# Kernel tuning notes

Measured on AMD Instinct MI355X. Metric: run time of the kernel, lower is better.

The kernel has to match this reference:

```python
import jax, jax.numpy as jnp
import numpy as np

DIM = 256
M = 100000
B = 1024
TOP_K = 32
N_HEADS = 4
EPS = 1e-8  # torch F.cosine_similarity eps


def setup_inputs() -> dict:
    key = jax.random.key(0)
    ks = jax.random.split(key, 8)
    return {
        "query": jax.random.normal(ks[0], (B, DIM), dtype=jnp.float32),
        "mem_keys": jax.random.normal(ks[1], (M, DIM), dtype=jnp.float32),
        "mem_values": jax.random.normal(ks[2], (M, DIM), dtype=jnp.float32),
        "W_q": jax.random.normal(ks[3], (DIM, DIM), dtype=jnp.float32) * 0.1,
        "in_proj_w": jax.random.normal(ks[4], (3 * DIM, DIM), dtype=jnp.float32) * 0.05,
        "in_proj_b": jax.random.normal(ks[5], (3 * DIM,), dtype=jnp.float32) * 0.05,
        "out_proj_w": jax.random.normal(ks[6], (DIM, DIM), dtype=jnp.float32) * 0.05,
        "out_proj_b": jax.random.normal(ks[7], (DIM,), dtype=jnp.float32) * 0.05,
    }


def reference(query, mem_keys, mem_values, W_q, in_proj_w, in_proj_b, out_proj_w, out_proj_b):
    b, d = query.shape
    hd = d // N_HEADS

    # projected query used both for retrieval and as attention query
    qt = query @ W_q  # [B, D]

    # batched cosine similarity against the whole bank
    qn = qt / jnp.maximum(jnp.linalg.norm(qt, axis=-1, keepdims=True), EPS)
    kn = mem_keys / jnp.maximum(jnp.linalg.norm(mem_keys, axis=-1, keepdims=True), EPS)
    sims = qn @ kn.T  # [B, M]  -- memory-bound stage

    _, idx = jax.lax.top_k(sims, TOP_K)  # [B, K]
    rk = mem_keys[idx]    # [B, K, D]
    rv = mem_values[idx]  # [B, K, D]

    # nn.MultiheadAttention math (batch_first, q_len=1, kv_len=K)
    Wq, Wk, Wv = jnp.split(in_proj_w, 3, axis=0)
    bq, bk, bv = jnp.split(in_proj_b, 3)
    q = qt @ Wq.T + bq                # [B, D]
    k = rk @ Wk.T + bk                # [B, K, D]
    v = rv @ Wv.T + bv                # [B, K, D]

    qh = q.reshape(b, N_HEADS, hd)                      # [B, H, hd]
    kh = k.reshape(b, TOP_K, N_HEADS, hd)               # [B, K, H, hd]
    vh = v.reshape(b, TOP_K, N_HEADS, hd)

    scores = jnp.einsum('bhd,bkhd->bhk', qh, kh) / jnp.sqrt(jnp.float32(hd))
    attn = jax.nn.softmax(scores, axis=-1)              # [B, H, K]
    out = jnp.einsum('bhk,bkhd->bhd', attn, vh).reshape(b, d)
    return out @ out_proj_w.T + out_proj_b              # [B, D]
```

## Files before the change

kernel.cpp:

```cpp
#include <hip/hip_runtime.h>
#include <hip/hip_bf16.h>

#define BQ 1024
#define DIMD 256
#define MKEYS 100000
#define TOPK 32
#define NSUPER 3125
#define PAIR_CAP 1024
#define EBUF_CAP 320
#define WKOFF (DIMD * DIMD)
#define WVOFF (2 * DIMD * DIMD)

typedef __attribute__((ext_vector_type(8))) short bf16x8;
typedef __attribute__((ext_vector_type(4))) float f32x4;

#define MFMA_16x16x32(a, b, c) __builtin_amdgcn_mfma_f32_16x16x32_bf16(a, b, c, 0, 0, 0)

__global__ __launch_bounds__(256) void k_zero(int* __restrict__ cnt) {
    const int i = blockIdx.x * 256 + threadIdx.x;
    if (i < BQ) cnt[i] = 0;
}

__global__ __launch_bounds__(256) void k_qt(const float* __restrict__ query,
                                            const float* __restrict__ Wq,
                                            float* __restrict__ qt,
                                            __hip_bfloat16* __restrict__ qtb,
                                            float* __restrict__ emit_thr) {
    __shared__ float qrow[DIMD];
    __shared__ float red[256];
    const int b = blockIdx.x, t = threadIdx.x;
    qrow[t] = query[b * DIMD + t];
    __syncthreads();
    float acc = 0.f;
#pragma unroll 4
    for (int k = 0; k < DIMD; ++k)
        acc = fmaf(qrow[k], Wq[k * DIMD + t], acc);
    qt[b * DIMD + t] = acc;
    qtb[b * DIMD + t] = __float2bfloat16(acc);
    red[t] = acc * acc;
    __syncthreads();
    for (int s = 128; s > 0; s >>= 1) {
        if (t < s) red[t] += red[t + s];
        __syncthreads();
    }
    if (t == 0) {
        const float sigma = sqrtf(red[0]) * (1.0f / 16.0f);
        emit_thr[b] = 3.0f * sigma - 0.02f;
    }
}

__global__ __launch_bounds__(256) void k_kn(const float* __restrict__ keys,
                                            __hip_bfloat16* __restrict__ knb,
                                            float* __restrict__ invn) {
    const int wv = threadIdx.x >> 6, lane = threadIdx.x & 63;
    const int row = blockIdx.x * 4 + wv;
    const float4 v = *(const float4*)(keys + (size_t)row * DIMD + lane * 4);
    float ss = v.x * v.x + v.y * v.y + v.z * v.z + v.w * v.w;
#pragma unroll
    for (int m = 1; m < 64; m <<= 1) ss += __shfl_xor(ss, m);
    const float inv = 1.0f / fmaxf(sqrtf(ss), 1e-8f);
    ushort4 u;
    u.x = (unsigned short)__builtin_bit_cast(short, __float2bfloat16(v.x * inv));
    u.y = (unsigned short)__builtin_bit_cast(short, __float2bfloat16(v.y * inv));
    u.z = (unsigned short)__builtin_bit_cast(short, __float2bfloat16(v.z * inv));
    u.w = (unsigned short)__builtin_bit_cast(short, __float2bfloat16(v.w * inv));
    *(ushort4*)((unsigned short*)knb + (size_t)row * DIMD + lane * 4) = u;
    if (lane == 0) invn[row] = inv;
}

__global__ __launch_bounds__(256) void k_tr(const float* __restrict__ in_w,
                                            const float* __restrict__ ow,
                                            float* __restrict__ wqT,
                                            float* __restrict__ owT) {
    __shared__ float tile[32][33];
    const int m = blockIdx.z;
    const float* src = (m == 0) ? in_w : ow;
    float* dst = (m == 0) ? wqT : owT;
    const int r0 = blockIdx.y * 32, c0 = blockIdx.x * 32;
    const int tr = threadIdx.x >> 5, tc = threadIdx.x & 31;
#pragma unroll
    for (int i = 0; i < 32; i += 8)
        tile[tr + i][tc] = src[(size_t)(r0 + tr + i) * DIMD + c0 + tc];
    __syncthreads();
#pragma unroll
    for (int i = 0; i < 32; i += 8)
        dst[(size_t)(c0 + tr + i) * DIMD + r0 + tc] = tile[tc][tr + i];
}

__global__ __launch_bounds__(256) void k_comb(const float* __restrict__ in_w,
                                              const float* __restrict__ in_b,
                                              const float* __restrict__ ob,
                                              const float* __restrict__ wqT,
                                              const float* __restrict__ owT,
                                              float* __restrict__ CombG,
                                              float* __restrict__ gbias,
                                              float* __restrict__ CombO,
                                              float* __restrict__ obias) {
    const int t = threadIdx.x;
    const int bid = blockIdx.x;
    if (bid < 256) {
        __shared__ float qe[DIMD];
        qe[t] = wqT[bid * DIMD + t];
        __syncthreads();
#pragma unroll
        for (int h = 0; h < 4; ++h) {
            float acc = 0.f;
#pragma unroll 4
            for (int d = 0; d < 64; ++d)
                acc = fmaf(qe[h * 64 + d], in_w[WKOFF + (size_t)(h * 64 + d) * DIMD + t], acc);
            CombG[(size_t)bid * 1024 + h * 256 + t] = acc;
        }
    } else if (bid < 1280) {
        const int hc = bid - 256;
        const int h = hc >> 8, c = hc & 255;
        float acc = 0.f;
#pragma unroll 4
        for (int d = 0; d < 64; ++d) {
            const int tt = h * 64 + d;
            acc = fmaf(in_w[WVOFF + (size_t)tt * DIMD + c], owT[(size_t)tt * DIMD + t], acc);
        }
        CombO[(size_t)hc * DIMD + t] = acc;
    } else if (bid == 1280) {
#pragma unroll
        for (int h = 0; h < 4; ++h) {
            float acc = 0.f;
#pragma unroll 4
            for (int d = 0; d < 64; ++d)
                acc = fmaf(in_b[h * 64 + d], in_w[WKOFF + (size_t)(h * 64 + d) * DIMD + t], acc);
            gbias[h * 256 + t] = acc;
        }
    } else {
        float acc = ob[t];
#pragma unroll 4
        for (int tt = 0; tt < DIMD; ++tt)
            acc = fmaf(in_b[2 * DIMD + tt], owT[(size_t)tt * DIMD + t], acc);
        obias[t] = acc;
    }
}

__global__ __launch_bounds__(256, 3) void k_sims(const __hip_bfloat16* __restrict__ qtb,
                                                 const __hip_bfloat16* __restrict__ knb,
                                                 const float* __restrict__ emit_thr,
                                                 int* __restrict__ cnt,
                                                 int2* __restrict__ pairs)
{
    __shared__ __align__(16) unsigned char btile[32 * 512];
    __shared__ float sthr[128];
    __shared__ int epack[EBUF_CAP];
    __shared__ float escore[EBUF_CAP];
    __shared__ int ebc;

    const int t = threadIdx.x;
    const int lane = t & 63;
    const int wv = t >> 6;
    const int col = lane & 15;
    const int quad = lane >> 4;
    const int xch = blockIdx.x >> 3;
    const int ych = blockIdx.x & 7;
    const int row0 = ych * 128;
    const int rloc_base = wv * 32;

    if (t < 128) sthr[t] = emit_thr[row0 + t];
    if (t == 0) ebc = 0;
    __syncthreads();

    float thr[2][4];
#pragma unroll
    for (int sub = 0; sub < 2; ++sub)
#pragma unroll
        for (int reg = 0; reg < 4; ++reg)
            thr[sub][reg] = sthr[rloc_base + sub * 16 + quad * 4 + reg];

    bf16x8 afr[2][8];
#pragma unroll
    for (int sub = 0; sub < 2; ++sub) {
        const short* ap = (const short*)qtb + (size_t)(row0 + rloc_base + sub * 16 + col) * DIMD;
#pragma unroll
        for (int kk = 0; kk < 8; ++kk)
            afr[sub][kk] = *(const bf16x8*)(ap + kk * 32 + quad * 8);
    }

    const int fm = t & 31;
    const int fr0 = t >> 5;

    const int st0 = xch * 25;
    const int st1 = st0 + 25;

    bf16x8 stg[4];
    {
        const char* gp = (const char*)knb + (size_t)st0 * 32 * 512;
#pragma unroll
        for (int it = 0; it < 4; ++it) {
            const int r = it * 8 + fr0;
            stg[it] = *(const bf16x8*)(gp + r * 512 + fm * 16);
        }
    }

    for (int st = st0; st < st1; ++st) {
        __syncthreads();
#pragma unroll
        for (int it = 0; it < 4; ++it) {
            const int r = it * 8 + fr0;
            *(bf16x8*)(btile + r * 512 + ((fm ^ (r & 7)) * 16)) = stg[it];
        }
        __syncthreads();

        if (st + 1 < st1) {
            const char* gp = (const char*)knb + (size_t)(st + 1) * 32 * 512;
#pragma unroll
            for (int it = 0; it < 4; ++it) {
                const int r = it * 8 + fr0;
                stg[it] = *(const bf16x8*)(gp + r * 512 + fm * 16);
            }
        }

        const int c0 = st * 32;
        f32x4 acc[2][2];
#pragma unroll
        for (int i = 0; i < 2; ++i)
#pragma unroll
            for (int j = 0; j < 2; ++j) { acc[i][j][0] = 0.f; acc[i][j][1] = 0.f; acc[i][j][2] = 0.f; acc[i][j][3] = 0.f; }

#pragma unroll
        for (int kt = 0; kt < 2; ++kt) {
            const int n = kt * 16 + col;
            const unsigned char* bp = btile + n * 512;
            const int nx = n & 7;
#pragma unroll
            for (int kk = 0; kk < 8; ++kk) {
                const int m = kk * 4 + quad;
                const bf16x8 b = *(const bf16x8*)(bp + ((m ^ nx) * 16));
                acc[0][kt] = MFMA_16x16x32(afr[0][kk], b, acc[0][kt]);
                acc[1][kt] = MFMA_16x16x32(afr[1][kk], b, acc[1][kt]);
            }
        }

#pragma unroll
        for (int sub = 0; sub < 2; ++sub) {
#pragma unroll
            for (int kt = 0; kt < 2; ++kt) {
#pragma unroll
                for (int reg = 0; reg < 4; ++reg) {
                    const float s = acc[sub][kt][reg];
                    if (s >= thr[sub][reg]) {
                        const int rl = rloc_base + sub * 16 + quad * 4 + reg;
                        const int key = c0 + kt * 16 + col;
                        const int p = atomicAdd(&ebc, 1);
                        if (p < EBUF_CAP) {
                            epack[p] = (rl << 17) | key;
                            escore[p] = s;
                        }
                    }
                }
            }
        }
    }

    __syncthreads();
    const int ne = min(ebc, EBUF_CAP);
    for (int i = t; i < ne; i += 256) {
        const int pk = epack[i];
        const int row = row0 + (pk >> 17);
        const int key = pk & 0x1FFFF;
        const int p = atomicAdd(&cnt[row], 1);
        if (p < PAIR_CAP)
            pairs[(size_t)row * PAIR_CAP + p] = make_int2(key, __float_as_int(escore[i]));
    }
}

__global__ __launch_bounds__(256) void k_pick(const int* __restrict__ cnt,
                                              const int2* __restrict__ pairs,
                                              const float* __restrict__ qt,
                                              const float* __restrict__ keys,
                                              const float* __restrict__ invn,
                                              int* __restrict__ topk) {
    __shared__ float sval[PAIR_CAP];
    __shared__ int skey[PAIR_CAP];
    __shared__ float qs[DIMD];
    __shared__ float wex[64];
    __shared__ int widx[64];
    __shared__ int wcnt;
    __shared__ float t32s;

    const int t = threadIdx.x;
    const int row = blockIdx.x;
    const int wv = t >> 6, lane = t & 63;

    qs[t] = qt[row * DIMD + t];
    const int n = min(cnt[row], PAIR_CAP);
    for (int i = t; i < n; i += 256) {
        int2 p = pairs[(size_t)row * PAIR_CAP + i];
        skey[i] = p.x;
        sval[i] = __int_as_float(p.y);
    }
    if (t == 0) { wcnt = 0; t32s = -1e30f; }
    __syncthreads();

    const int target = min(31, n - 1);
    for (int i = t; i < n; i += 256) {
        const float v = sval[i];
        const int k = skey[i];
        int r = 0;
        for (int j = 0; j < n; ++j) {
            const float vj = sval[j];
            r += (vj > v) || (vj == v && skey[j] < k);
        }
        if (r == target) t32s = v;
    }
    __syncthreads();
    const float t32 = t32s;

    for (int i = t; i < n; i += 256)
        if (sval[i] >= t32 - 0.04f) {
            int p = atomicAdd(&wcnt, 1);
            if (p < 64) widx[p] = skey[i];
        }
    __syncthreads();
    const int wn = min(wcnt, 64);

    for (int c = wv; c < wn; c += 4) {
        const int key = widx[c];
        const float4 kv = ((const float4*)(keys + (size_t)key * DIMD))[lane];
        float s = kv.x * qs[lane * 4] + kv.y * qs[lane * 4 + 1] +
                  kv.z * qs[lane * 4 + 2] + kv.w * qs[lane * 4 + 3];
#pragma unroll
        for (int m = 1; m < 64; m <<= 1) s += __shfl_xor(s, m);
        if (lane == 0) wex[c] = s * invn[key];
    }
    __syncthreads();

    if (t < 64) {
        const bool have = t < wn;
        const float v = have ? wex[t] : -1e30f;
        const int k = have ? widx[t] : 0x7FFFFFFF;
        int r = 0;
        for (int j = 0; j < wn; ++j) {
            const float vj = wex[j];
            r += (vj > v) || (vj == v && widx[j] < k);
        }
        const bool sel = have && (r < TOPK);
        const unsigned long long mask = __ballot(sel);
        if (sel) {
            const int pos = __popcll(mask & ((1ull << t) - 1));
            topk[row * TOPK + pos] = k;
        }
        if (t == 0) {
            const int tot = __popcll(mask);
            for (int z = tot; z < TOPK; ++z) topk[row * TOPK + z] = 0;
        }
    }
}

__global__ __launch_bounds__(256) void k_g(const float* __restrict__ qt,
                                           const float* __restrict__ CombG,
                                           const float* __restrict__ gbias,
                                           float* __restrict__ G) {
    __shared__ __align__(16) float qts[8][264];
    const int t = threadIdx.x;
    const int b0 = blockIdx.x * 8;
    const int c0 = blockIdx.y * 512 + t;
    const int c1 = c0 + 256;

#pragma unroll
    for (int r = 0; r < 8; ++r) qts[r][t] = qt[(size_t)(b0 + r) * DIMD + t];
    __syncthreads();

    float acc0[8], acc1[8];
#pragma unroll
    for (int r = 0; r < 8; ++r) { acc0[r] = 0.f; acc1[r] = 0.f; }

    for (int e = 0; e < DIMD; e += 4) {
        float4 qf[8];
#pragma unroll
        for (int r = 0; r < 8; ++r) qf[r] = *(const float4*)&qts[r][e];
#pragma unroll
        for (int j = 0; j < 4; ++j) {
            const float w0 = CombG[(size_t)(e + j) * 1024 + c0];
            const float w1 = CombG[(size_t)(e + j) * 1024 + c1];
#pragma unroll
            for (int r = 0; r < 8; ++r) {
                const float qv = (j == 0) ? qf[r].x : (j == 1) ? qf[r].y : (j == 2) ? qf[r].z : qf[r].w;
                acc0[r] = fmaf(qv, w0, acc0[r]);
                acc1[r] = fmaf(qv, w1, acc1[r]);
            }
        }
    }

    const float gb0 = gbias[c0 & 1023];
    const float gb1 = gbias[c1 & 1023];
#pragma unroll
    for (int r = 0; r < 8; ++r) {
        G[(size_t)(b0 + r) * 1024 + c0] = acc0[r] + gb0;
        G[(size_t)(b0 + r) * 1024 + c1] = acc1[r] + gb1;
    }
}

__global__ __launch_bounds__(256) void k_att(const float* __restrict__ G,
                                             const float* __restrict__ mem_keys,
                                             const float* __restrict__ mem_values,
                                             const int* __restrict__ topk,
                                             float* __restrict__ rvbar) {
    __shared__ float gs[4 * DIMD];
    __shared__ __align__(16) float ktile[32 * 264];
    __shared__ float at[4][TOPK];

    const int t = threadIdx.x;
    const int b = blockIdx.x;
    const int gr = t >> 3, gc = t & 7;

    int idx = topk[b * TOPK + gr];
    idx = ((unsigned)idx < MKEYS) ? idx : 0;
    const float4* kp = (const float4*)(mem_keys + (size_t)idx * DIMD);
    const float4* vp = (const float4*)(mem_values + (size_t)idx * DIMD);

    float4 sk[8], sv[8];
#pragma unroll
    for (int i = 0; i < 8; ++i) sk[i] = kp[gc + 8 * i];
    const float4 g4 = ((const float4*)G)[(size_t)b * 256 + t];
#pragma unroll
    for (int i = 0; i < 8; ++i) sv[i] = vp[gc + 8 * i];

    ((float4*)gs)[t] = g4;
    {
        float* kd = ktile + gr * 264;
#pragma unroll
        for (int i = 0; i < 8; ++i)
            *(float4*)(kd + ((gc ^ (gr & 7)) + 8 * i) * 4) = sk[i];
    }
    __syncthreads();

    const int h = t >> 6;
    const int s = (t >> 1) & 31;
    const int half = t & 1;
    {
        const float* kr = ktile + s * 264;
        const float* gp = gs + h * DIMD + half * 128;
        float4 a4 = {0.f, 0.f, 0.f, 0.f};
#pragma unroll
        for (int j = 0; j < 32; ++j) {
            const int l = half * 32 + j;
            const int phys = ((l & 7) ^ (s & 7)) | (l & 56);
            const float4 kv = *(const float4*)(kr + phys * 4);
            const float4 gv = *(const float4*)(gp + j * 4);
            a4.x = fmaf(kv.x, gv.x, a4.x);
            a4.y = fmaf(kv.y, gv.y, a4.y);
            a4.z = fmaf(kv.z, gv.z, a4.z);
            a4.w = fmaf(kv.w, gv.w, a4.w);
        }
        float a = (a4.x + a4.y) + (a4.z + a4.w);
        a += __shfl_xor(a, 1);
        a *= 0.125f;
        float mx = a;
#pragma unroll
        for (int m = 32; m >= 1; m >>= 1) mx = fmaxf(mx, __shfl_xor(mx, m));
        const float e = __expf(a - mx);
        float sum = e;
#pragma unroll
        for (int m = 32; m >= 1; m >>= 1) sum += __shfl_xor(sum, m);
        at[h][s] = (e + e) / sum;
    }
    __syncthreads();

    {
        float* kd = ktile + gr * 264;
#pragma unroll
        for (int i = 0; i < 8; ++i)
            *(float4*)(kd + ((gc ^ (gr & 7)) + 8 * i) * 4) = sv[i];
    }
    __syncthreads();

    {
        float a0 = 0.f, a1 = 0.f, a2 = 0.f, a3 = 0.f;
        const int l = t >> 2, w = t & 3;
#pragma unroll
        for (int k = 0; k < TOPK; ++k) {
            const int phys = ((l & 7) ^ (k & 7)) | (l & 56);
            const float v = ktile[k * 264 + phys * 4 + w];
            a0 = fmaf(at[0][k], v, a0);
            a1 = fmaf(at[1][k], v, a1);
            a2 = fmaf(at[2][k], v, a2);
            a3 = fmaf(at[3][k], v, a3);
        }
        float* rp = rvbar + (size_t)b * 1024;
        rp[t] = a0;
        rp[256 + t] = a1;
        rp[512 + t] = a2;
        rp[768 + t] = a3;
    }
}

__global__ __launch_bounds__(256) void k_out(const float* __restrict__ rvbar,
                                             const float* __restrict__ CombO,
                                             const float* __restrict__ obias,
                                             float* __restrict__ out) {
    __shared__ __align__(16) float rvs[4][1024];
    const int t = threadIdx.x;
    const int b0 = blockIdx.x * 4;

#pragma unroll
    for (int r = 0; r < 4; ++r)
#pragma unroll
        for (int i = 0; i < 4; ++i)
            rvs[r][t + 256 * i] = rvbar[(size_t)(b0 + r) * 1024 + t + 256 * i];
    __syncthreads();

    float acc[4];
#pragma unroll
    for (int r = 0; r < 4; ++r) acc[r] = 0.f;

#pragma unroll 2
    for (int k = 0; k < 1024; k += 4) {
        float4 qf[4];
#pragma unroll
        for (int r = 0; r < 4; ++r) qf[r] = *(const float4*)&rvs[r][k];
#pragma unroll
        for (int j = 0; j < 4; ++j) {
            const float w = CombO[(size_t)(k + j) * DIMD + t];
#pragma unroll
            for (int r = 0; r < 4; ++r) {
                const float qv = (j == 0) ? qf[r].x : (j == 1) ? qf[r].y : (j == 2) ? qf[r].z : qf[r].w;
                acc[r] = fmaf(qv, w, acc[r]);
            }
        }
    }

    const float obt = obias[t];
#pragma unroll
    for (int r = 0; r < 4; ++r)
        out[(size_t)(b0 + r) * DIMD + t] = acc[r] + obt;
}

extern "C" void kernel_launch(void* const* d_in, const int* in_sizes, int n_in,
                              void* d_out, int out_size, void* d_ws, size_t ws_size,
                              hipStream_t stream) {
    const float* query = (const float*)d_in[0];
    const float* mem_keys = (const float*)d_in[1];
    const float* mem_values = (const float*)d_in[2];
    const float* Wq = (const float*)d_in[3];
    const float* in_w = (const float*)d_in[4];
    const float* in_b = (const float*)d_in[5];
    const float* ow = (const float*)d_in[6];
    const float* ob = (const float*)d_in[7];
    float* out = (float*)d_out;

    char* ws = (char*)d_ws;
    size_t off = 0;
    auto alloc = [&](size_t bytes) -> void* {
        void* p = ws + off;
        off = (off + bytes + 255) & ~(size_t)255;
        return p;
    };
    __hip_bfloat16* knb = (__hip_bfloat16*)alloc((size_t)MKEYS * DIMD * 2);
    float* invn = (float*)alloc((size_t)MKEYS * 4);
    float* qt = (float*)alloc((size_t)BQ * DIMD * 4);
    __hip_bfloat16* qtb = (__hip_bfloat16*)alloc((size_t)BQ * DIMD * 2);
    float* emit_thr = (float*)alloc((size_t)BQ * 4);
    int* cnt = (int*)alloc((size_t)BQ * 4);
    int2* pairs = (int2*)alloc((size_t)BQ * PAIR_CAP * 8);
    int* topk = (int*)alloc((size_t)BQ * TOPK * 4);
    float* wqT = (float*)alloc((size_t)DIMD * DIMD * 4);
    float* owT = (float*)alloc((size_t)DIMD * DIMD * 4);
    float* CombG = (float*)alloc((size_t)DIMD * 1024 * 4);
    float* CombO = (float*)alloc((size_t)1024 * DIMD * 4);
    float* gbias = (float*)alloc((size_t)1024 * 4);
    float* obias = (float*)alloc((size_t)DIMD * 4);
    float* G = (float*)alloc((size_t)BQ * 1024 * 4);
    float* rvbar = (float*)alloc((size_t)BQ * 1024 * 4);

    k_zero<<<(BQ + 255) / 256, 256, 0, stream>>>(cnt);
    k_qt<<<BQ, 256, 0, stream>>>(query, Wq, qt, qtb, emit_thr);
    k_kn<<<MKEYS / 4, 256, 0, stream>>>(mem_keys, knb, invn);
    {
        dim3 gt(8, 8, 2);
        k_tr<<<gt, 256, 0, stream>>>(in_w, ow, wqT, owT);
    }
    k_comb<<<1282, 256, 0, stream>>>(in_w, in_b, ob, wqT, owT, CombG, gbias, CombO, obias);
    k_sims<<<1000, 256, 0, stream>>>(qtb, knb, emit_thr, cnt, pairs);
    k_pick<<<BQ, 256, 0, stream>>>(cnt, pairs, qt, mem_keys, invn, topk);
    {
        dim3 gg(128, 2);
        k_g<<<gg, 256, 0, stream>>>(qt, CombG, gbias, G);
    }
    k_att<<<BQ, 256, 0, stream>>>(G, mem_keys, mem_values, topk, rvbar);
    k_out<<<BQ / 4, 256, 0, stream>>>(rvbar, CombO, obias, out);
}
```

Baseline: 477.9 us.

## Drop zero and transpose kernels, remap sims blocks for XCD locality

Folds the counter zeroing into k_qt and removes the weight-transpose kernel. k_comb now reads in_w and ow directly, using shared staging and float4 loads. Both changes cut two launches and their intermediate buffers. k_sims is launched with 1024 blocks and remaps block IDs so that consecutive key chunks land on the same XCD, with surplus blocks exiting early, to improve L2 reuse of key tiles across the row chunks. The risk is strided, uncoalesced reads of in_w in k_comb's first branch and a few idle blocks.

```diff
diff --git a/kernel.cpp b/kernel.cpp
--- a/kernel.cpp
+++ b/kernel.cpp
@@ -16,19 +16,16 @@
 
 #define MFMA_16x16x32(a, b, c) __builtin_amdgcn_mfma_f32_16x16x32_bf16(a, b, c, 0, 0, 0)
 
-__global__ __launch_bounds__(256) void k_zero(int* __restrict__ cnt) {
-    const int i = blockIdx.x * 256 + threadIdx.x;
-    if (i < BQ) cnt[i] = 0;
-}
-
 __global__ __launch_bounds__(256) void k_qt(const float* __restrict__ query,
                                             const float* __restrict__ Wq,
                                             float* __restrict__ qt,
                                             __hip_bfloat16* __restrict__ qtb,
-                                            float* __restrict__ emit_thr) {
+                                            float* __restrict__ emit_thr,
+                                            int* __restrict__ cnt) {
     __shared__ float qrow[DIMD];
     __shared__ float red[256];
     const int b = blockIdx.x, t = threadIdx.x;
+    if (t == 0) cnt[b] = 0;
     qrow[t] = query[b * DIMD + t];
     __syncthreads();
     float acc = 0.f;
@@ -68,30 +65,10 @@
     if (lane == 0) invn[row] = inv;
 }
 
-__global__ __launch_bounds__(256) void k_tr(const float* __restrict__ in_w,
-                                            const float* __restrict__ ow,
-                                            float* __restrict__ wqT,
-                                            float* __restrict__ owT) {
-    __shared__ float tile[32][33];
-    const int m = blockIdx.z;
-    const float* src = (m == 0) ? in_w : ow;
-    float* dst = (m == 0) ? wqT : owT;
-    const int r0 = blockIdx.y * 32, c0 = blockIdx.x * 32;
-    const int tr = threadIdx.x >> 5, tc = threadIdx.x & 31;
-#pragma unroll
-    for (int i = 0; i < 32; i += 8)
-        tile[tr + i][tc] = src[(size_t)(r0 + tr + i) * DIMD + c0 + tc];
-    __syncthreads();
-#pragma unroll
-    for (int i = 0; i < 32; i += 8)
-        dst[(size_t)(c0 + tr + i) * DIMD + r0 + tc] = tile[tc][tr + i];
-}
-
 __global__ __launch_bounds__(256) void k_comb(const float* __restrict__ in_w,
                                               const float* __restrict__ in_b,
                                               const float* __restrict__ ob,
-                                              const float* __restrict__ wqT,
-                                              const float* __restrict__ owT,
+                                              const float* __restrict__ ow,
                                               float* __restrict__ CombG,
                                               float* __restrict__ gbias,
                                               float* __restrict__ CombO,
@@ -100,7 +77,7 @@
     const int bid = blockIdx.x;
     if (bid < 256) {
         __shared__ float qe[DIMD];
-        qe[t] = wqT[bid * DIMD + t];
+        qe[t] = in_w[(size_t)t * DIMD + bid];
         __syncthreads();
 #pragma unroll
         for (int h = 0; h < 4; ++h) {
@@ -113,11 +90,18 @@
     } else if (bid < 1280) {
         const int hc = bid - 256;
         const int h = hc >> 8, c = hc & 255;
+        __shared__ float wvc[64];
+        if (t < 64) wvc[t] = in_w[WVOFF + (size_t)(h * 64 + t) * DIMD + c];
+        __syncthreads();
+        const float4* owp = (const float4*)(ow + (size_t)t * DIMD + h * 64);
         float acc = 0.f;
-#pragma unroll 4
-        for (int d = 0; d < 64; ++d) {
-            const int tt = h * 64 + d;
-            acc = fmaf(in_w[WVOFF + (size_t)tt * DIMD + c], owT[(size_t)tt * DIMD + t], acc);
+#pragma unroll
+        for (int i = 0; i < 16; ++i) {
+            const float4 o4 = owp[i];
+            acc = fmaf(wvc[4 * i], o4.x, acc);
+            acc = fmaf(wvc[4 * i + 1], o4.y, acc);
+            acc = fmaf(wvc[4 * i + 2], o4.z, acc);
+            acc = fmaf(wvc[4 * i + 3], o4.w, acc);
         }
         CombO[(size_t)hc * DIMD + t] = acc;
     } else if (bid == 1280) {
@@ -130,10 +114,19 @@
             gbias[h * 256 + t] = acc;
         }
     } else {
+        __shared__ float bv[DIMD];
+        bv[t] = in_b[2 * DIMD + t];
+        __syncthreads();
+        const float4* owp = (const float4*)(ow + (size_t)t * DIMD);
         float acc = ob[t];
 #pragma unroll 4
-        for (int tt = 0; tt < DIMD; ++tt)
-            acc = fmaf(in_b[2 * DIMD + tt], owT[(size_t)tt * DIMD + t], acc);
+        for (int i = 0; i < 64; ++i) {
+            const float4 o4 = owp[i];
+            acc = fmaf(bv[4 * i], o4.x, acc);
+            acc = fmaf(bv[4 * i + 1], o4.y, acc);
+            acc = fmaf(bv[4 * i + 2], o4.z, acc);
+            acc = fmaf(bv[4 * i + 3], o4.w, acc);
+        }
         obias[t] = acc;
     }
 }
@@ -150,13 +143,18 @@
     __shared__ float escore[EBUF_CAP];
     __shared__ int ebc;
 
+    const int id = blockIdx.x;
+    const int xcd = id & 7;
+    const int q = id >> 3;
+    const int ych = q & 7;
+    const int xch = (q >> 3) * 8 + xcd;
+    if (xch >= 125) return;
+
     const int t = threadIdx.x;
     const int lane = t & 63;
     const int wv = t >> 6;
     const int col = lane & 15;
     const int quad = lane >> 4;
-    const int xch = blockIdx.x >> 3;
-    const int ych = blockIdx.x & 7;
     const int row0 = ych * 128;
     const int rloc_base = wv * 32;
 
@@ -558,8 +556,6 @@
     int* cnt = (int*)alloc((size_t)BQ * 4);
     int2* pairs = (int2*)alloc((size_t)BQ * PAIR_CAP * 8);
     int* topk = (int*)alloc((size_t)BQ * TOPK * 4);
-    float* wqT = (float*)alloc((size_t)DIMD * DIMD * 4);
-    float* owT = (float*)alloc((size_t)DIMD * DIMD * 4);
     float* CombG = (float*)alloc((size_t)DIMD * 1024 * 4);
     float* CombO = (float*)alloc((size_t)1024 * DIMD * 4);
     float* gbias = (float*)alloc((size_t)1024 * 4);
@@ -567,15 +563,10 @@
     float* G = (float*)alloc((size_t)BQ * 1024 * 4);
     float* rvbar = (float*)alloc((size_t)BQ * 1024 * 4);
 
-    k_zero<<<(BQ + 255) / 256, 256, 0, stream>>>(cnt);
-    k_qt<<<BQ, 256, 0, stream>>>(query, Wq, qt, qtb, emit_thr);
+    k_qt<<<BQ, 256, 0, stream>>>(query, Wq, qt, qtb, emit_thr, cnt);
     k_kn<<<MKEYS / 4, 256, 0, stream>>>(mem_keys, knb, invn);
-    {
-        dim3 gt(8, 8, 2);
-        k_tr<<<gt, 256, 0, stream>>>(in_w, ow, wqT, owT);
-    }
-    k_comb<<<1282, 256, 0, stream>>>(in_w, in_b, ob, wqT, owT, CombG, gbias, CombO, obias);
-    k_sims<<<1000, 256, 0, stream>>>(qtb, knb, emit_thr, cnt, pairs);
+    k_comb<<<1282, 256, 0, stream>>>(in_w, in_b, ob, ow, CombG, gbias, CombO, obias);
+    k_sims<<<1024, 256, 0, stream>>>(qtb, knb, emit_thr, cnt, pairs);
     k_pick<<<BQ, 256, 0, stream>>>(cnt, pairs, qt, mem_keys, invn, topk);
     {
         dim3 gg(128, 2);
```

New measurement: 463.1 us. 1.03x faster.
